# Kernel tuning notes

Measured on AMD Instinct MI355X. Metric: run time of the kernel, lower is better.

The kernel has to match this reference:

```python
import jax, jax.numpy as jnp
import numpy as np

DIM = 512
HEADS = 8
DIM_HEAD = 64
INNER = HEADS * DIM_HEAD  # 512
B, N = 4, 2048
EPS = 1e-5
DIFF = 1.0


def setup_inputs() -> dict:
    key = jax.random.key(0)
    ks = jax.random.split(key, 8)
    s = 1.0 / np.sqrt(DIM)
    return {
        "x": jax.random.normal(ks[0], (B, N, DIM), dtype=jnp.float32),
        "ln_w": jnp.ones((DIM,), jnp.float32),
        "ln_b": jnp.zeros((DIM,), jnp.float32),
        "wq": jax.random.uniform(ks[1], (INNER, DIM), jnp.float32, -s, s),
        "wk": jax.random.uniform(ks[2], (INNER, DIM), jnp.float32, -s, s),
        "wv_v": jax.random.uniform(ks[3], (INNER, DIM), jnp.float32, -s, s),  # weight-norm direction
        "wv_g": jax.random.uniform(ks[4], (INNER,), jnp.float32, 0.5, 1.5),   # weight-norm magnitude g
        "w_out": jax.random.uniform(ks[5], (DIM, INNER), jnp.float32, -s, s),
    }


def reference(x, ln_w, ln_b, wq, wk, wv_v, wv_g, w_out):
    # LayerNorm over last dim
    mu = jnp.mean(x, axis=-1, keepdims=True)
    var = jnp.mean(jnp.square(x - mu), axis=-1, keepdims=True)
    xn = (x - mu) * jax.lax.rsqrt(var + EPS) * ln_w + ln_b

    # weight-norm for V projection: W = g * v / ||v||_row (norm over dim=1)
    wv = wv_g[:, None] * wv_v / jnp.linalg.norm(wv_v, axis=1, keepdims=True)

    def proj(w):  # [b n (h d)] -> [b h n d]
        t = jnp.einsum('bnc,ec->bne', xn, w)
        return t.reshape(x.shape[0], x.shape[1], HEADS, DIM_HEAD).transpose(0, 2, 1, 3)

    q, k, v = proj(wq), proj(wk), proj(wv)

    scale = DIM_HEAD ** -0.5
    dots = jnp.einsum('bhid,bhjd->bhij', q, k) * scale
    attn = jax.nn.softmax(dots, axis=-1)
    out = jnp.einsum('bhij,bhjd->bhid', DIFF * attn, v)  # diff-scaled AV
    out = out.transpose(0, 2, 1, 3).reshape(x.shape[0], x.shape[1], INNER)
    return jnp.einsum('bne,ce->bnc', out, w_out)
```

## Files before the change

kernel.cpp:

```cpp
#include <hip/hip_runtime.h>
#include <hip/hip_bf16.h>
#include <stdint.h>

typedef __attribute__((ext_vector_type(8))) __bf16 bf16x8;
typedef __attribute__((ext_vector_type(8))) short short8;
typedef __attribute__((ext_vector_type(4))) float f32x4;

#define C1_QSCALE 0.18033688011112042f

__device__ __forceinline__ unsigned short f2bf(float f) {
    union { float f; unsigned int u; } v; v.f = f;
    unsigned int r = v.u + 0x7fffu + ((v.u >> 16) & 1u);
    return (unsigned short)(r >> 16);
}

__device__ __forceinline__ unsigned int cvtpk(float lo, float hi) {
    unsigned int r;
    asm("v_cvt_pk_bf16_f32 %0, %1, %2" : "=v"(r) : "v"(lo), "v"(hi));
    return r;
}

__device__ __forceinline__ float fexp2(float x) {
    float r;
    asm("v_exp_f32 %0, %1" : "=v"(r) : "v"(x));
    return r;
}

__device__ __forceinline__ void gl_lds16(const void* g, void* l) {
    __builtin_amdgcn_global_load_lds(
        (const __attribute__((address_space(1))) unsigned int*)g,
        (__attribute__((address_space(3))) unsigned int*)l, 16, 0, 0);
}

__device__ __forceinline__ f32x4 mfma16(bf16x8 a, bf16x8 b, f32x4 c) {
    return __builtin_amdgcn_mfma_f32_16x16x32_bf16(a, b, c, 0, 0, 0);
}

__global__ __launch_bounds__(256) void pre_kernel(
    const float* __restrict__ x, const float* __restrict__ lw,
    const float* __restrict__ lb, unsigned short* __restrict__ xn,
    const float* __restrict__ wq, const float* __restrict__ wk,
    const float* __restrict__ wv_v, const float* __restrict__ wv_g,
    const float* __restrict__ w_out,
    unsigned short* __restrict__ wqkv, unsigned short* __restrict__ woutb)
{
    const int t = threadIdx.x;
    if (blockIdx.x < 2048) {
        const int wv = t >> 6, l = t & 63;
        const int row = blockIdx.x * 4 + wv;
        const float* xr = x + (size_t)row * 512;
        const float4 a = *(const float4*)(xr + l*8);
        const float4 b = *(const float4*)(xr + l*8 + 4);
        float s  = (a.x + a.y) + (a.z + a.w) + (b.x + b.y) + (b.z + b.w);
        float sq = (a.x*a.x + a.y*a.y) + (a.z*a.z + a.w*a.w)
                 + (b.x*b.x + b.y*b.y) + (b.z*b.z + b.w*b.w);
        #pragma unroll
        for (int m = 1; m < 64; m <<= 1) { s += __shfl_xor(s, m); sq += __shfl_xor(sq, m); }
        const float mean = s * (1.f/512.f);
        const float var  = sq * (1.f/512.f) - mean*mean;
        const float rs   = rsqrtf(var + 1e-5f);
        const float4 w0 = *(const float4*)(lw + l*8);
        const float4 w1 = *(const float4*)(lw + l*8 + 4);
        const float4 c0 = *(const float4*)(lb + l*8);
        const float4 c1 = *(const float4*)(lb + l*8 + 4);
        uint4 o;
        o.x = cvtpk((a.x-mean)*rs*w0.x + c0.x, (a.y-mean)*rs*w0.y + c0.y);
        o.y = cvtpk((a.z-mean)*rs*w0.z + c0.z, (a.w-mean)*rs*w0.w + c0.w);
        o.z = cvtpk((b.x-mean)*rs*w1.x + c1.x, (b.y-mean)*rs*w1.y + c1.y);
        o.w = cvtpk((b.z-mean)*rs*w1.z + c1.z, (b.w-mean)*rs*w1.w + c1.w);
        *(uint4*)(xn + (size_t)row*512 + l*8) = o;
    } else {
        __shared__ float red[4];
        const int row = blockIdx.x - 2048;
        if (row < 1536) {
            const float* src;
            float scale = 1.0f;
            if (row < 512) src = wq + (size_t)row*512;
            else if (row < 1024) src = wk + (size_t)(row-512)*512;
            else {
                src = wv_v + (size_t)(row-1024)*512;
                float2 v = *(const float2*)(src + t*2);
                float sq = v.x*v.x + v.y*v.y;
                #pragma unroll
                for (int m = 1; m < 64; m <<= 1) sq += __shfl_xor(sq, m);
                if ((t & 63) == 0) red[t >> 6] = sq;
                __syncthreads();
                scale = wv_g[row-1024] * rsqrtf(red[0]+red[1]+red[2]+red[3]);
            }
            float2 v = *(const float2*)(src + t*2);
            ushort2 o; o.x = f2bf(v.x*scale); o.y = f2bf(v.y*scale);
            *(ushort2*)(wqkv + (size_t)row*512 + t*2) = o;
        } else {
            const int r = row - 1536;
            float2 v = *(const float2*)(w_out + (size_t)r*512 + t*2);
            ushort2 o; o.x = f2bf(v.x); o.y = f2bf(v.y);
            *(ushort2*)(woutb + (size_t)r*512 + t*2) = o;
        }
    }
}

template<int MODE, int BM, int BN>
__global__ __launch_bounds__(256) void gemm_nt(
    const unsigned short* __restrict__ A,
    const unsigned short* __restrict__ B,
    unsigned short* __restrict__ qo,
    unsigned short* __restrict__ ko,
    unsigned short* __restrict__ vo,
    float* __restrict__ outf)
{
    constexpr int MT = BM / 32;
    constexpr int NT = BN / 32;
    __shared__ __align__(16) unsigned char As[2][BM*128];
    __shared__ __align__(16) unsigned char Bs[2][BN*128];
    const int t = threadIdx.x;
    const int wv = t >> 6, l = t & 63;
    const int brow = blockIdx.x * BM;
    const int bcol = blockIdx.y * BN;
    const int wr = (wv >> 1) * (BM/2), wc = (wv & 1) * (BN/2);
    const int l15 = l & 15, l4 = l >> 4;
    const int rl = l >> 3, cbl = l & 7;

    const f32x4 fz = {0.f, 0.f, 0.f, 0.f};
    f32x4 acc[MT][NT];
    #pragma unroll
    for (int i = 0; i < MT; ++i)
        #pragma unroll
        for (int j = 0; j < NT; ++j) acc[i][j] = fz;

    auto STAGE = [&](int ks, int buf) {
        #pragma unroll
        for (int i = 0; i < MT; ++i) {
            const int c = wv*MT + i;
            const int row = c*8 + rl;
            const int scb = cbl ^ (row & 7);
            gl_lds16(A + (size_t)(brow+row)*512 + ks*64 + scb*8, &As[buf][c*1024]);
        }
        #pragma unroll
        for (int i = 0; i < NT; ++i) {
            const int c = wv*NT + i;
            const int row = c*8 + rl;
            const int scb = cbl ^ (row & 7);
            gl_lds16(B + (size_t)(bcol+row)*512 + ks*64 + scb*8, &Bs[buf][c*1024]);
        }
    };

    STAGE(0, 0);
    asm volatile("s_waitcnt vmcnt(0)" ::: "memory");
    __syncthreads();

    int cur = 0;
    for (int ks = 0; ks < 8; ++ks) {
        if (ks < 7) STAGE(ks + 1, cur ^ 1);
        #pragma unroll
        for (int kk = 0; kk < 2; ++kk) {
            bf16x8 af[MT], bfr[NT];
            #pragma unroll
            for (int mt = 0; mt < MT; ++mt) {
                const int row = wr + mt*16 + l15;
                const int cb = kk*4 + l4;
                af[mt] = *(const bf16x8*)(&As[cur][0] + row*128 + ((cb ^ (row & 7))*16));
            }
            #pragma unroll
            for (int nt = 0; nt < NT; ++nt) {
                const int row = wc + nt*16 + l15;
                const int cb = kk*4 + l4;
                bfr[nt] = *(const bf16x8*)(&Bs[cur][0] + row*128 + ((cb ^ (row & 7))*16));
            }
            __builtin_amdgcn_s_setprio(1);
            #pragma unroll
            for (int mt = 0; mt < MT; ++mt)
                #pragma unroll
                for (int nt = 0; nt < NT; ++nt)
                    acc[mt][nt] = mfma16(af[mt], bfr[nt], acc[mt][nt]);
            __builtin_amdgcn_s_setprio(0);
        }
        asm volatile("s_waitcnt vmcnt(0)" ::: "memory");
        __syncthreads();
        cur ^= 1;
    }

    if (MODE == 1) {
        #pragma unroll
        for (int mt = 0; mt < MT; ++mt)
            #pragma unroll
            for (int nt = 0; nt < NT; ++nt)
                #pragma unroll
                for (int r = 0; r < 4; ++r) {
                    const int grow = brow + wr + mt*16 + l4*4 + r;
                    const int gcol = bcol + wc + nt*16 + l15;
                    outf[(size_t)grow*512 + gcol] = acc[mt][nt][r];
                }
    } else if (bcol < 1024) {
        const bool isq = (bcol < 512);
        unsigned short* dst = isq ? qo : ko;
        const int csub = isq ? bcol : bcol - 512;
        const float scl = isq ? C1_QSCALE : 1.0f;
        #pragma unroll
        for (int mt = 0; mt < MT; ++mt)
            #pragma unroll
            for (int nt = 0; nt < NT; ++nt)
                #pragma unroll
                for (int r = 0; r < 4; ++r) {
                    const int grow = brow + wr + mt*16 + l4*4 + r;
                    const int gcol = csub + wc + nt*16 + l15;
                    const int h = gcol >> 6, d = gcol & 63;
                    const int bb = grow >> 11, n = grow & 2047;
                    dst[(((size_t)bb*8 + h)*2048 + n)*64 + d] = f2bf(acc[mt][nt][r]*scl);
                }
    } else {
        #pragma unroll
        for (int mt = 0; mt < MT; ++mt) {
            const int grow0 = brow + wr + mt*16 + l4*4;
            const int bb = grow0 >> 11;
            const int nb = (grow0 & 2047) & ~63;
            const int sigma0 = (mt>>1)*32 + l4*8 + (mt&1)*4;
            #pragma unroll
            for (int nt = 0; nt < NT; ++nt) {
                const int gcol = (bcol - 1024) + wc + nt*16 + l15;
                const int h = gcol >> 6, d = gcol & 63;
                uint2 ov;
                ov.x = cvtpk(acc[mt][nt][0], acc[mt][nt][1]);
                ov.y = cvtpk(acc[mt][nt][2], acc[mt][nt][3]);
                *(uint2*)(vo + ((size_t)(bb*8 + h)*64 + d)*2048 + nb + sigma0) = ov;
            }
        }
    }
}

__global__ __launch_bounds__(256, 4) void flash_attn(
    const unsigned short* __restrict__ Q,
    const unsigned short* __restrict__ K,
    const unsigned short* __restrict__ Vt,
    unsigned short* __restrict__ AO)
{
    __shared__ __align__(16) unsigned char Ks[3][8192];
    __shared__ __align__(16) unsigned char Vs[2][8192];
    const int t = threadIdx.x, wv = t >> 6, l = t & 63;
    const int l15 = l & 15, l4 = l >> 4;
    const int rl = l >> 3, cbl = l & 7;
    const int bh = blockIdx.x;
    const int q0 = blockIdx.y * 64;
    const size_t base = (size_t)bh * 2048 * 64;
    const int b = bh >> 3, h = bh & 7;

    bf16x8 qf[2];
    #pragma unroll
    for (int kk = 0; kk < 2; ++kk)
        qf[kk] = *(const bf16x8*)(Q + base + (size_t)(q0 + wv*16 + l15)*64 + kk*32 + 8*l4);

    const f32x4 fz = {0.f,0.f,0.f,0.f};
    f32x4 acco[4];
    float lrp = 0.f;
    #pragma unroll
    for (int dn = 0; dn < 4; ++dn) acco[dn] = fz;

    auto STAGE_K = [&](int kv, int buf) {
        #pragma unroll
        for (int i = 0; i < 2; ++i) {
            const int c = wv*2 + i;
            const int row = c*8 + rl;
            const int scb = cbl ^ (row & 7);
            gl_lds16(K + base + (size_t)(kv + row)*64 + scb*8, &Ks[buf][c*1024]);
        }
    };
    auto STAGE_V = [&](int kv, int buf) {
        #pragma unroll
        for (int i = 0; i < 2; ++i) {
            const int c = wv*2 + i;
            const int row = c*8 + rl;
            const int scb = cbl ^ (row & 7);
            gl_lds16(Vt + base + (size_t)row*2048 + kv + scb*8, &Vs[buf][c*1024]);
        }
    };

    STAGE_V(0, 0);
    STAGE_K(0, 0);
    STAGE_K(64, 1);

    int kb = 0, vb = 0;
    for (int it = 0; it < 32; ++it) {
        asm volatile("s_waitcnt vmcnt(2)" ::: "memory");
        __builtin_amdgcn_s_barrier();

        STAGE_V(((it + 1) & 31) * 64, vb ^ 1);
        STAGE_K(((it + 2) & 31) * 64, kb >= 1 ? kb - 1 : 2);

        bf16x8 kf[4][2];
        #pragma unroll
        for (int nt = 0; nt < 4; ++nt)
            #pragma unroll
            for (int kk = 0; kk < 2; ++kk) {
                const int row = nt*16 + l15;
                const int cb = kk*4 + l4;
                kf[nt][kk] = *(const bf16x8*)(&Ks[kb][0] + row*128 + ((cb ^ (row & 7))*16));
            }
        f32x4 st[4];
        __builtin_amdgcn_s_setprio(1);
        #pragma unroll
        for (int nt = 0; nt < 4; ++nt) {
            st[nt] = mfma16(kf[nt][0], qf[0], fz);
            st[nt] = mfma16(kf[nt][1], qf[1], st[nt]);
        }
        __builtin_amdgcn_s_setprio(0);

        float p[4][4];
        #pragma unroll
        for (int nt = 0; nt < 4; ++nt)
            #pragma unroll
            for (int r = 0; r < 4; ++r) p[nt][r] = fexp2(st[nt][r]);
        float s0 = (p[0][0]+p[0][1]) + (p[0][2]+p[0][3]);
        float s1 = (p[1][0]+p[1][1]) + (p[1][2]+p[1][3]);
        float s2 = (p[2][0]+p[2][1]) + (p[2][2]+p[2][3]);
        float s3 = (p[3][0]+p[3][1]) + (p[3][2]+p[3][3]);
        lrp += (s0 + s1) + (s2 + s3);

        bf16x8 pb[2];
        #pragma unroll
        for (int kh = 0; kh < 2; ++kh) {
            union { unsigned int u[4]; bf16x8 v; } pu;
            pu.u[0] = cvtpk(p[2*kh][0],   p[2*kh][1]);
            pu.u[1] = cvtpk(p[2*kh][2],   p[2*kh][3]);
            pu.u[2] = cvtpk(p[2*kh+1][0], p[2*kh+1][1]);
            pu.u[3] = cvtpk(p[2*kh+1][2], p[2*kh+1][3]);
            pb[kh] = pu.v;
        }

        __builtin_amdgcn_s_setprio(1);
        #pragma unroll
        for (int dn = 0; dn < 4; ++dn)
            #pragma unroll
            for (int kh = 0; kh < 2; ++kh) {
                const int row = dn*16 + l15;
                const int cb = kh*4 + l4;
                const bf16x8 vf = *(const bf16x8*)(&Vs[vb][0] + row*128 + ((cb ^ (row & 7))*16));
                acco[dn] = mfma16(vf, pb[kh], acco[dn]);
            }
        __builtin_amdgcn_s_setprio(0);

        kb = (kb == 2) ? 0 : kb + 1;
        vb ^= 1;
    }

    float lr = lrp;
    lr += __shfl_xor(lr, 16);
    lr += __shfl_xor(lr, 32);
    const float inv = 1.f / lr;
    const size_t nrow = (size_t)b*2048 + q0 + wv*16 + l15;
    #pragma unroll
    for (int dn = 0; dn < 4; ++dn) {
        uint2 ov;
        ov.x = cvtpk(acco[dn][0]*inv, acco[dn][1]*inv);
        ov.y = cvtpk(acco[dn][2]*inv, acco[dn][3]*inv);
        *(uint2*)(AO + nrow*512 + h*64 + dn*16 + l4*4) = ov;
    }
}

extern "C" void kernel_launch(void* const* d_in, const int* in_sizes, int n_in,
                              void* d_out, int out_size, void* d_ws, size_t ws_size,
                              hipStream_t stream)
{
    const float* x     = (const float*)d_in[0];
    const float* ln_w  = (const float*)d_in[1];
    const float* ln_b  = (const float*)d_in[2];
    const float* wq    = (const float*)d_in[3];
    const float* wk    = (const float*)d_in[4];
    const float* wv_v  = (const float*)d_in[5];
    const float* wv_g  = (const float*)d_in[6];
    const float* w_out = (const float*)d_in[7];
    float* out = (float*)d_out;
    char* ws = (char*)d_ws;

    unsigned short* xn    = (unsigned short*)(ws);
    unsigned short* ao    = (unsigned short*)(ws);
    unsigned short* wqkv  = (unsigned short*)(ws +  8388608);
    unsigned short* woutb = (unsigned short*)(ws +  9961472);
    unsigned short* q     = (unsigned short*)(ws + 10485760);
    unsigned short* k     = (unsigned short*)(ws + 18874368);
    unsigned short* vt    = (unsigned short*)(ws + 27262976);

    pre_kernel<<<dim3(4096), dim3(256), 0, stream>>>(x, ln_w, ln_b, xn,
        wq, wk, wv_v, wv_g, w_out, wqkv, woutb);
    gemm_nt<0,128,128><<<dim3(64, 12), dim3(256), 0, stream>>>(xn, wqkv, q, k, vt, (float*)nullptr);
    flash_attn<<<dim3(32, 32), dim3(256), 0, stream>>>(q, k, vt, ao);
    gemm_nt<1,128,64><<<dim3(64, 8), dim3(256), 0, stream>>>(ao, woutb,
        (unsigned short*)nullptr, (unsigned short*)nullptr, (unsigned short*)nullptr, out);
}
```

Before: 160.1 us.

## Triple-buffer GEMM K-loop with 32-wide slices and partial vmcnt waits

Restructures the bf16 NT GEMM mainloop into a three-stage LDS ring of 32-wide K slices, replacing the double-buffered 64-wide slices. Prefetch runs two stages ahead, and each iteration waits only for the oldest loads via a partial vmcnt count plus a single barrier, so global loads overlap with MFMA work. The LDS swizzle is changed to a 4-chunk XOR pattern to match the 64-byte rows. This doubles the number of barriers per K pass, and the steady-state loop issues redundant wrap-around loads in its last two iterations.

```diff
diff --git a/kernel.cpp b/kernel.cpp
--- a/kernel.cpp
+++ b/kernel.cpp
@@ -108,17 +108,21 @@
     unsigned short* __restrict__ vo,
     float* __restrict__ outf)
 {
-    constexpr int MT = BM / 32;
-    constexpr int NT = BN / 32;
-    __shared__ __align__(16) unsigned char As[2][BM*128];
-    __shared__ __align__(16) unsigned char Bs[2][BN*128];
+    constexpr int MT  = BM / 32;
+    constexpr int NT  = BN / 32;
+    constexpr int ACH = BM / 64;
+    constexpr int BCH = BN / 64;
+    constexpr int BUFSZ = (BM + BN) * 64;
+    __shared__ __align__(16) unsigned char L[3][BUFSZ];
+
     const int t = threadIdx.x;
     const int wv = t >> 6, l = t & 63;
     const int brow = blockIdx.x * BM;
     const int bcol = blockIdx.y * BN;
     const int wr = (wv >> 1) * (BM/2), wc = (wv & 1) * (BN/2);
     const int l15 = l & 15, l4 = l >> 4;
-    const int rl = l >> 3, cbl = l & 7;
+    const int rl  = l >> 2;
+    const int cbl = l & 3;
 
     const f32x4 fz = {0.f, 0.f, 0.f, 0.f};
     f32x4 acc[MT][NT];
@@ -129,54 +133,53 @@
 
     auto STAGE = [&](int ks, int buf) {
         #pragma unroll
-        for (int i = 0; i < MT; ++i) {
-            const int c = wv*MT + i;
-            const int row = c*8 + rl;
-            const int scb = cbl ^ (row & 7);
-            gl_lds16(A + (size_t)(brow+row)*512 + ks*64 + scb*8, &As[buf][c*1024]);
-        }
-        #pragma unroll
-        for (int i = 0; i < NT; ++i) {
-            const int c = wv*NT + i;
-            const int row = c*8 + rl;
-            const int scb = cbl ^ (row & 7);
-            gl_lds16(B + (size_t)(bcol+row)*512 + ks*64 + scb*8, &Bs[buf][c*1024]);
+        for (int i = 0; i < ACH; ++i) {
+            const int c = wv*ACH + i;
+            const int row = c*16 + rl;
+            const int scb = cbl ^ ((row >> 1) & 3);
+            gl_lds16(A + (size_t)(brow+row)*512 + ks*32 + scb*8, &L[buf][c*1024]);
+        }
+        #pragma unroll
+        for (int i = 0; i < BCH; ++i) {
+            const int c = wv*BCH + i;
+            const int row = c*16 + rl;
+            const int scb = cbl ^ ((row >> 1) & 3);
+            gl_lds16(B + (size_t)(bcol+row)*512 + ks*32 + scb*8, &L[buf][BM*64 + c*1024]);
         }
     };
 
     STAGE(0, 0);
-    asm volatile("s_waitcnt vmcnt(0)" ::: "memory");
-    __syncthreads();
+    STAGE(1, 1);
 
     int cur = 0;
-    for (int ks = 0; ks < 8; ++ks) {
-        if (ks < 7) STAGE(ks + 1, cur ^ 1);
-        #pragma unroll
-        for (int kk = 0; kk < 2; ++kk) {
-            bf16x8 af[MT], bfr[NT];
-            #pragma unroll
-            for (int mt = 0; mt < MT; ++mt) {
-                const int row = wr + mt*16 + l15;
-                const int cb = kk*4 + l4;
-                af[mt] = *(const bf16x8*)(&As[cur][0] + row*128 + ((cb ^ (row & 7))*16));
-            }
-            #pragma unroll
-            for (int nt = 0; nt < NT; ++nt) {
-                const int row = wc + nt*16 + l15;
-                const int cb = kk*4 + l4;
-                bfr[nt] = *(const bf16x8*)(&Bs[cur][0] + row*128 + ((cb ^ (row & 7))*16));
-            }
-            __builtin_amdgcn_s_setprio(1);
-            #pragma unroll
-            for (int mt = 0; mt < MT; ++mt)
-                #pragma unroll
-                for (int nt = 0; nt < NT; ++nt)
-                    acc[mt][nt] = mfma16(af[mt], bfr[nt], acc[mt][nt]);
-            __builtin_amdgcn_s_setprio(0);
-        }
-        asm volatile("s_waitcnt vmcnt(0)" ::: "memory");
-        __syncthreads();
-        cur ^= 1;
+    for (int ks = 0; ks < 16; ++ks) {
+        if constexpr (ACH + BCH == 4) asm volatile("s_waitcnt vmcnt(4)" ::: "memory");
+        else                          asm volatile("s_waitcnt vmcnt(3)" ::: "memory");
+        __builtin_amdgcn_s_barrier();
+
+        int nb = cur + 2; if (nb >= 3) nb -= 3;
+        STAGE((ks + 2) & 15, nb);
+
+        bf16x8 af[MT], bfr[NT];
+        #pragma unroll
+        for (int mt = 0; mt < MT; ++mt) {
+            const int row = wr + mt*16 + l15;
+            af[mt] = *(const bf16x8*)(&L[cur][0] + row*64 + ((l4 ^ ((row >> 1) & 3))*16));
+        }
+        #pragma unroll
+        for (int nt = 0; nt < NT; ++nt) {
+            const int row = wc + nt*16 + l15;
+            bfr[nt] = *(const bf16x8*)(&L[cur][BM*64] + row*64 + ((l4 ^ ((row >> 1) & 3))*16));
+        }
+        __builtin_amdgcn_s_setprio(1);
+        #pragma unroll
+        for (int mt = 0; mt < MT; ++mt)
+            #pragma unroll
+            for (int nt = 0; nt < NT; ++nt)
+                acc[mt][nt] = mfma16(af[mt], bfr[nt], acc[mt][nt]);
+        __builtin_amdgcn_s_setprio(0);
+
+        cur = (cur == 2) ? 0 : cur + 1;
     }
 
     if (MODE == 1) {
@@ -212,7 +215,7 @@
         for (int mt = 0; mt < MT; ++mt) {
             const int grow0 = brow + wr + mt*16 + l4*4;
             const int bb = grow0 >> 11;
-            const int nb = (grow0 & 2047) & ~63;
+            const int nb2 = (grow0 & 2047) & ~63;
             const int sigma0 = (mt>>1)*32 + l4*8 + (mt&1)*4;
             #pragma unroll
             for (int nt = 0; nt < NT; ++nt) {
@@ -221,7 +224,7 @@
                 uint2 ov;
                 ov.x = cvtpk(acc[mt][nt][0], acc[mt][nt][1]);
                 ov.y = cvtpk(acc[mt][nt][2], acc[mt][nt][3]);
-                *(uint2*)(vo + ((size_t)(bb*8 + h)*64 + d)*2048 + nb + sigma0) = ov;
+                *(uint2*)(vo + ((size_t)(bb*8 + h)*64 + d)*2048 + nb2 + sigma0) = ov;
             }
         }
     }
```

Result: no change. 157.3 us (-1.7%).
